# Kernel tuning notes

Measured on AMD Instinct MI355X. Metric: run time of the kernel, lower is better.

Reference implementation:

```python
import jax, jax.numpy as jnp
import numpy as np

B, L, D, H = 2, 1024, 1024, 16
HD = D // H           # 64 head dim
P = 2 * L - 1         # 2047 relative positions (covers offsets -(L-1)..L-1 with wrap)


def setup_inputs() -> dict:
    key = jax.random.key(0)
    ks = jax.random.split(key, 6)
    x = jax.random.normal(ks[0], (B, L, D), dtype=jnp.float32)
    # causal mask: True where attention is disallowed (masked_fill semantics)
    mask = jnp.triu(jnp.ones((L, L), dtype=bool), k=1)
    W_qkv = jax.random.normal(ks[1], (D, 3 * D), dtype=jnp.float32) * 0.02
    b_qkv = jnp.zeros((3 * D,), dtype=jnp.float32)
    W_o = jax.random.normal(ks[2], (D, D), dtype=jnp.float32) * 0.02
    b_o = jnp.zeros((D,), dtype=jnp.float32)
    Er = jax.random.normal(ks[3], (H, P, HD), dtype=jnp.float32)
    return {"x": x, "mask": mask, "W_qkv": W_qkv, "b_qkv": b_qkv,
            "W_o": W_o, "b_o": b_o, "Er": Er}


def reference(x, mask, W_qkv, b_qkv, W_o, b_o, Er):
    b, l, d = x.shape
    h, p, hd = Er.shape
    qkv = x @ W_qkv + b_qkv                              # [b, l, 3d]
    q, k, v = jnp.split(qkv, 3, axis=-1)
    q = q.reshape(b, l, h, hd).transpose(0, 2, 1, 3)     # [b, h, l, hd]
    k = k.reshape(b, l, h, hd).transpose(0, 2, 1, 3)
    v = v.reshape(b, l, h, hd).transpose(0, 2, 1, 3)

    scale = 1.0 / jnp.sqrt(jnp.float32(hd))
    a = jnp.einsum('bhid,bhjd->bhij', q, k) * scale      # [b, h, l, l]

    # relative-position bias: QEr[b,h,i,j] = sum_d q[b,h,i,d] * Er[h, (j-i)%p, d]
    # Efficient skew form: contract q with full table, then gather along last axis.
    QE = jnp.einsum('bhid,hpd->bhip', q, Er)             # [b, h, l, p]
    rel = (jnp.arange(l)[None, :] - jnp.arange(l)[:, None]) % p  # [l, l], matches torch neg-index wrap
    QEr = jnp.take_along_axis(QE, rel[None, None], axis=-1)      # [b, h, l, l]
    a = a + QEr

    a = jnp.where(mask, -jnp.inf, a)
    a = jax.nn.softmax(a, axis=-1)                        # dropout is identity in eval

    out = jnp.einsum('bhij,bhjd->bihd', a, v).reshape(b, l, d)
    return out @ W_o + b_o
```

## Files before the change

### kernel.cpp

```cpp
#include <hip/hip_runtime.h>

typedef _Float16 f16;
typedef _Float16 f16x8 __attribute__((ext_vector_type(8)));
typedef float f32x4 __attribute__((ext_vector_type(4)));

static_assert(sizeof(f16x8) == 16, "f16x8 must be 16B");

#define MFMA16x16x32F(a, b, c) __builtin_amdgcn_mfma_f32_16x16x32_f16((a), (b), (c), 0, 0, 0)

#define NB 2
#define NL 1024
#define ND 1024
#define NH 16
#define NHD 64
#define NP 2047
#define NBH (NB * NH)

__device__ __forceinline__ void wave_sync_lds() {
  __builtin_amdgcn_sched_barrier(0);
  asm volatile("s_waitcnt lgkmcnt(0)" ::: "memory");
  __builtin_amdgcn_sched_barrier(0);
}

__device__ __forceinline__ void gload16(const f16* g, f16* lds) {
  __builtin_amdgcn_global_load_lds((const __attribute__((address_space(1))) void*)g,
                                   (__attribute__((address_space(3))) void*)lds, 16, 0, 0);
}

__global__ __launch_bounds__(256) void prep_all_k(const float* __restrict__ er,
                                                  f16* __restrict__ epf,
                                                  const float* __restrict__ x,
                                                  f16* __restrict__ xf,
                                                  const float* __restrict__ Wqkv,
                                                  f16* __restrict__ WTqkv,
                                                  const float* __restrict__ Wo,
                                                  f16* __restrict__ WTo) {
  const int b = blockIdx.x;
  const int t = threadIdx.x;
  if (b < 8192) {
    const int i = b * 256 + t;
    const int e = i & 7;
    const int lane = (i >> 3) & 63;
    const int half = (i >> 9) & 1;
    const int ob = (i >> 10) & 127;
    const int h = i >> 17;
    const int g = lane >> 4, cl = lane & 15;
    const int o = ob * 16 - 1024 + cl;
    const int p = (o <= 0) ? -o : (NP - o);
    const int d = half * 32 + g * 8 + e;
    epf[i] = (f16)er[(size_t)(h * NP + p) * NHD + d];
  } else if (b < 16384) {
    const int i = (b - 8192) * 256 + t;
    xf[i] = (f16)x[i];
  } else {
    __shared__ float tile[64][68];
    const int b2 = b - 16384;
    const int bx = b2 >> 4;
    const int k0 = (b2 & 15) * 64;
    const float* W;
    f16* WT;
    int N, n0;
    if (bx < 48) { W = Wqkv; WT = WTqkv; N = 3072; n0 = bx * 64; }
    else         { W = Wo;   WT = WTo;   N = 1024; n0 = (bx - 48) * 64; }
    const int rc = t & 15;
    const int rr0 = t >> 4;
#pragma unroll
    for (int i = 0; i < 4; ++i) {
      const int row = rr0 + i * 16;
      float4 v = *(const float4*)(W + (size_t)(k0 + row) * N + n0 + rc * 4);
      *(float4*)&tile[row][rc * 4] = v;
    }
    __syncthreads();
    const int n = t >> 2, kc = (t & 3) * 16;
    f16x8 h0, h1;
#pragma unroll
    for (int e = 0; e < 8; ++e) h0[e] = (f16)tile[kc + e][n];
#pragma unroll
    for (int e = 0; e < 8; ++e) h1[e] = (f16)tile[kc + 8 + e][n];
    f16* dst = WT + (size_t)(n0 + n) * ND + k0 + kc;
    *(f16x8*)dst = h0;
    *(f16x8*)(dst + 8) = h1;
  }
}

__global__ __launch_bounds__(256) void qkv_gemm_k(const f16* __restrict__ Xf,
                                                  const f16* __restrict__ WT,
                                                  const float* __restrict__ bias,
                                                  f16* __restrict__ qf,
                                                  f16* __restrict__ kp, f16* __restrict__ vp) {
  __shared__ f16 sA[2][64 * 32], sB[2][128 * 32];
  const int t = threadIdx.x;
  const int lane = t & 63;
  const int w = t >> 6;
  const int cl = lane & 15;
  const int g = lane >> 4;
  const int m0 = blockIdx.y * 64;
  const int n0 = blockIdx.x * 128;

  const int arow = w * 16 + (lane >> 2);
  const int brow0 = w * 32 + (lane >> 2);
  const int scol = ((lane & 3) ^ ((lane >> 3) & 3)) * 8;
  const int rsw = (g ^ ((cl >> 1) & 3)) * 8;

  f32x4 acc[4][2] = {};

  for (int k0 = 0; k0 < ND; k0 += 64) {
#pragma unroll
    for (int kc = 0; kc < 2; ++kc) {
      const int kk = k0 + kc * 32;
      gload16(Xf + (size_t)(m0 + arow) * ND + kk + scol, &sA[kc][w * 512]);
      const f16* gb0 = WT + (size_t)(n0 + brow0) * ND + kk + scol;
      gload16(gb0, &sB[kc][w * 1024]);
      gload16(gb0 + (size_t)16 * ND, &sB[kc][w * 1024 + 512]);
    }
    __syncthreads();

#pragma unroll
    for (int kc = 0; kc < 2; ++kc) {
      f16x8 ah[4], bh[2];
#pragma unroll
      for (int fm = 0; fm < 4; ++fm) ah[fm] = *(const f16x8*)&sA[kc][(fm * 16 + cl) * 32 + rsw];
#pragma unroll
      for (int fn = 0; fn < 2; ++fn) bh[fn] = *(const f16x8*)&sB[kc][(w * 32 + fn * 16 + cl) * 32 + rsw];
#pragma unroll
      for (int fm = 0; fm < 4; ++fm)
#pragma unroll
        for (int fn = 0; fn < 2; ++fn)
          acc[fm][fn] = MFMA16x16x32F(ah[fm], bh[fn], acc[fm][fn]);
    }
    __syncthreads();
  }

#pragma unroll
  for (int fm = 0; fm < 4; ++fm) {
#pragma unroll
    for (int fn = 0; fn < 2; ++fn) {
#pragma unroll
      for (int reg = 0; reg < 4; ++reg) {
        const int gm = m0 + fm * 16 + g * 4 + reg;
        const int gn = n0 + w * 32 + fn * 16 + cl;
        float val = acc[fm][fn][reg] + bias[gn];
        const int bb = gm >> 10, lpos = gm & 1023;
        const int sec = gn >> 10, hc = gn & 1023;
        const int hh = hc >> 6, dd = hc & 63;
        const int bh = bb * NH + hh;
        if (sec == 0) {
          qf[(size_t)(bh * NL + lpos) * NHD + dd] = (f16)val;
        } else if (sec == 1) {
          const size_t idx = ((size_t)((bh * 64 + (lpos >> 4)) * 2 + (dd >> 5))) * 512 +
                             ((((dd >> 3) & 3) << 4) + (lpos & 15)) * 8 + (dd & 7);
          kp[idx] = (f16)val;
        } else {
          const size_t idx = ((size_t)(((bh * 16 + (lpos >> 6)) * 4 + (dd >> 4)) * 2 +
                                       ((lpos >> 5) & 1))) * 512 +
                             ((((lpos >> 3) & 3) << 4) + (dd & 15)) * 8 + (lpos & 7);
          vp[idx] = (f16)val;
        }
      }
    }
  }
}

__global__ __launch_bounds__(256) void attn_k(const f16* __restrict__ qf,
                                              const f16* __restrict__ kp, const f16* __restrict__ vp,
                                              const f16* __restrict__ epf,
                                              f16* __restrict__ ao) {
  __shared__ float s_lds[4][16][67];
  __shared__ float mb[4][16], lbuf[4][16], linv[16];

  const int t = threadIdx.x;
  const int w = t >> 6;
  const int lane = t & 63;
  const int cl = lane & 15;
  const int g = lane >> 4;

  const int n = blockIdx.x;
  const int xcd = n & 7, idx = n >> 3;
  const int bh = (xcd << 2) | (idx >> 6);
  const int itile = 63 - (idx & 63);
  const int i0 = itile * 16;
  const int h = bh & (NH - 1);
  const int nchunks = (itile >> 2) + 1;

  const f16* qfb = qf + (size_t)(bh * NL + i0 + cl) * NHD + g * 8;
  const f16x8 q_f0 = *(const f16x8*)qfb;
  const f16x8 q_f1 = *(const f16x8*)(qfb + 32);

  f32x4 acc_o[4] = {};
  float m_s = -3e38f, l_s = 0.0f;

  for (int jc = w; jc < nchunks; jc += 4) {
    const int j0 = jc * 64;
    const int delta = i0 - j0;

    const f16* vbase = vp + ((size_t)(bh * 16 + (j0 >> 6)) * 8) * 512 + lane * 8;
    f16x8 vf[4][2];
#pragma unroll
    for (int t4 = 0; t4 < 4; ++t4) {
      vf[t4][0] = *(const f16x8*)(vbase + (t4 * 2 + 0) * 512);
      vf[t4][1] = *(const f16x8*)(vbase + (t4 * 2 + 1) * 512);
    }

    const f16* kbase = kp + ((size_t)(bh * 64 + (j0 >> 4)) * 2) * 512 + lane * 8;
    f32x4 acc_s[4];
    __builtin_amdgcn_s_setprio(1);
#pragma unroll
    for (int jn = 0; jn < 4; ++jn) {
      f16x8 kf0 = *(const f16x8*)(kbase + (jn * 2 + 0) * 512);
      f16x8 kf1 = *(const f16x8*)(kbase + (jn * 2 + 1) * 512);
      f32x4 a = {};
      a = MFMA16x16x32F(q_f0, kf0, a);
      a = MFMA16x16x32F(q_f1, kf1, a);
      acc_s[jn] = a;
    }

    const int ob0 = (delta >> 4) + 60;
    const f16* ebase = epf + ((size_t)(h * 128 + ob0) * 2) * 512 + lane * 8;
    f32x4 acc_e[5];
#pragma unroll
    for (int tt = 0; tt < 5; ++tt) {
      f16x8 ef0 = *(const f16x8*)(ebase + (tt * 2 + 0) * 512);
      f16x8 ef1 = *(const f16x8*)(ebase + (tt * 2 + 1) * 512);
      f32x4 c = {};
      c = MFMA16x16x32F(q_f0, ef0, c);
      c = MFMA16x16x32F(q_f1, ef1, c);
      acc_e[tt] = c;
    }
    __builtin_amdgcn_s_setprio(0);

#pragma unroll
    for (int reg = 0; reg < 4; ++reg) {
      const int r = g * 4 + reg;
      const int src = (g << 4) | ((r - cl) & 15);
      const bool ge = (r >= cl);
#pragma unroll
      for (int jn = 0; jn < 4; ++jn) {
        float e_hi = __shfl(acc_e[4 - jn][reg], src);
        float e_lo = __shfl(acc_e[3 - jn][reg], src);
        s_lds[w][r][jn * 16 + cl] = fmaf(acc_s[jn][reg], 0.125f, ge ? e_hi : e_lo);
      }
    }
    wave_sync_lds();

    float sv[16];
    float tmax = -3e38f;
#pragma unroll
    for (int cc = 0; cc < 16; ++cc) {
      const int c = (cc < 8) ? (g * 8 + cc) : (32 + g * 8 + (cc - 8));
      float v = s_lds[w][cl][c];
      if (c > delta + cl) v = -3e38f;
      sv[cc] = v;
      tmax = fmaxf(tmax, v);
    }
    tmax = fmaxf(tmax, __shfl_xor(tmax, 16));
    tmax = fmaxf(tmax, __shfl_xor(tmax, 32));
    const float m_new = fmaxf(m_s, tmax);
    const float fsc = __builtin_amdgcn_exp2f((m_s - m_new) * 1.44269504f);
    float psum = 0.0f;
    f16x8 pf0, pf1;
#pragma unroll
    for (int cc = 0; cc < 16; ++cc) {
      float pv = __builtin_amdgcn_exp2f((sv[cc] - m_new) * 1.44269504f);
      psum += pv;
      if (cc < 8) pf0[cc & 7] = (f16)pv;
      else        pf1[cc & 7] = (f16)pv;
    }
    psum += __shfl_xor(psum, 16);
    psum += __shfl_xor(psum, 32);
    l_s = l_s * fsc + psum;
    m_s = m_new;

    float fr[4];
#pragma unroll
    for (int reg = 0; reg < 4; ++reg) fr[reg] = __shfl(fsc, g * 4 + reg);
#pragma unroll
    for (int t4 = 0; t4 < 4; ++t4) {
#pragma unroll
      for (int reg = 0; reg < 4; ++reg) acc_o[t4][reg] *= fr[reg];
    }
    __builtin_amdgcn_s_setprio(1);
#pragma unroll
    for (int t4 = 0; t4 < 4; ++t4) {
      acc_o[t4] = MFMA16x16x32F(pf0, vf[t4][0], acc_o[t4]);
      acc_o[t4] = MFMA16x16x32F(pf1, vf[t4][1], acc_o[t4]);
    }
    __builtin_amdgcn_s_setprio(0);
  }

  if (lane < 16) {
    mb[w][lane] = m_s;
    lbuf[w][lane] = l_s;
  }
  __syncthreads();
  const float M = fmaxf(fmaxf(mb[0][cl], mb[1][cl]), fmaxf(mb[2][cl], mb[3][cl]));
  const float sc = __builtin_amdgcn_exp2f((m_s - M) * 1.44269504f);
  float Lt = 0.0f;
#pragma unroll
  for (int ww = 0; ww < 4; ++ww)
    Lt += lbuf[ww][cl] * __builtin_amdgcn_exp2f((mb[ww][cl] - M) * 1.44269504f);
  if (w == 0 && lane < 16) linv[lane] = 1.0f / Lt;
  float fr2[4];
#pragma unroll
  for (int reg = 0; reg < 4; ++reg) fr2[reg] = __shfl(sc, g * 4 + reg);
#pragma unroll
  for (int t4 = 0; t4 < 4; ++t4) {
#pragma unroll
    for (int reg = 0; reg < 4; ++reg)
      s_lds[w][g * 4 + reg][t4 * 16 + cl] = acc_o[t4][reg] * fr2[reg];
  }
  __syncthreads();
  const int bb = bh >> 4;
#pragma unroll
  for (int rep = 0; rep < 4; ++rep) {
    const int o_ = t + rep * 256;
    const int r = o_ >> 6, c = o_ & 63;
    float s = s_lds[0][r][c] + s_lds[1][r][c] + s_lds[2][r][c] + s_lds[3][r][c];
    ao[(size_t)(bb * NL + i0 + r) * ND + h * NHD + c] = (f16)(s * linv[r]);
  }
}

__global__ __launch_bounds__(256) void out_gemm_k(const f16* __restrict__ A,
                                                  const f16* __restrict__ WT,
                                                  const float* __restrict__ bias,
                                                  float* __restrict__ out) {
  __shared__ f16 sA[2][64 * 32], sB[2][128 * 32];
  const int t = threadIdx.x;
  const int lane = t & 63, w = t >> 6;
  const int cl = lane & 15, g = lane >> 4;
  const int m0 = blockIdx.x * 64;
  const int n0 = blockIdx.y * 128;

  const int arow = w * 16 + (lane >> 2);
  const int brow0 = w * 32 + (lane >> 2);
  const int scol = ((lane & 3) ^ ((lane >> 3) & 3)) * 8;
  const int rsw = (g ^ ((cl >> 1) & 3)) * 8;

  f32x4 acc[4][2] = {};

  for (int k0 = 0; k0 < ND; k0 += 64) {
#pragma unroll
    for (int kc = 0; kc < 2; ++kc) {
      const int kk = k0 + kc * 32;
      gload16(A + (size_t)(m0 + arow) * ND + kk + scol, &sA[kc][w * 512]);
      const f16* gb0 = WT + (size_t)(n0 + brow0) * ND + kk + scol;
      gload16(gb0, &sB[kc][w * 1024]);
      gload16(gb0 + (size_t)16 * ND, &sB[kc][w * 1024 + 512]);
    }
    __syncthreads();
#pragma unroll
    for (int kc = 0; kc < 2; ++kc) {
      f16x8 ah[4], bh[2];
#pragma unroll
      for (int fm = 0; fm < 4; ++fm) ah[fm] = *(const f16x8*)&sA[kc][(fm * 16 + cl) * 32 + rsw];
#pragma unroll
      for (int fn = 0; fn < 2; ++fn) bh[fn] = *(const f16x8*)&sB[kc][(w * 32 + fn * 16 + cl) * 32 + rsw];
#pragma unroll
      for (int fm = 0; fm < 4; ++fm)
#pragma unroll
        for (int fn = 0; fn < 2; ++fn)
          acc[fm][fn] = MFMA16x16x32F(ah[fm], bh[fn], acc[fm][fn]);
    }
    __syncthreads();
  }
#pragma unroll
  for (int fm = 0; fm < 4; ++fm) {
#pragma unroll
    for (int fn = 0; fn < 2; ++fn) {
#pragma unroll
      for (int reg = 0; reg < 4; ++reg) {
        const int gm = m0 + fm * 16 + g * 4 + reg;
        const int gn = n0 + w * 32 + fn * 16 + cl;
        out[(size_t)gm * ND + gn] = acc[fm][fn][reg] + bias[gn];
      }
    }
  }
}

extern "C" void kernel_launch(void* const* d_in, const int* in_sizes, int n_in,
                              void* d_out, int out_size, void* d_ws, size_t ws_size,
                              hipStream_t stream) {
  (void)in_sizes; (void)n_in; (void)out_size; (void)ws_size;
  const float* x = (const float*)d_in[0];
  const float* Wqkv = (const float*)d_in[2];
  const float* bqkv = (const float*)d_in[3];
  const float* Wo = (const float*)d_in[4];
  const float* bo = (const float*)d_in[5];
  const float* Er = (const float*)d_in[6];

  char* ws = (char*)d_ws;
  size_t off = 0;
  auto take = [&](size_t bytes) {
    char* p = ws + off;
    off += (bytes + 255) & ~(size_t)255;
    return p;
  };
  const size_t qkN = (size_t)NBH * NL * NHD;
  const size_t xN = (size_t)NB * NL * ND;
  const size_t erpN = (size_t)NH * 128 * 2 * 512;
  f16* epf = (f16*)take(erpN * 2);
  f16* qfw = (f16*)take(qkN * 2);
  f16* kpw = (f16*)take(qkN * 2);
  f16* vpw = (f16*)take(qkN * 2);
  f16* wqkvt = (f16*)take((size_t)3 * ND * ND * 2);
  f16* wot   = (f16*)take((size_t)ND * ND * 2);
  f16* xf    = (f16*)take(xN * 2);
  f16* aow = wqkvt;

  prep_all_k<<<17408, 256, 0, stream>>>(Er, epf, x, xf, Wqkv, wqkvt, Wo, wot);
  qkv_gemm_k<<<dim3(24, 32), 256, 0, stream>>>(xf, wqkvt, bqkv, qfw, kpw, vpw);
  attn_k<<<2048, 256, 0, stream>>>(qfw, kpw, vpw, epf, aow);
  out_gemm_k<<<dim3(32, 8), 256, 0, stream>>>(aow, wot, bo, (float*)d_out);
}
```

Measured before the change: 85.55 us.

## Process two 16-row query tiles per attention block to reuse K/V/Er loads

Each attention block now handles 32 query rows as two 16-row tiles, so every K, V and relative-position fragment loaded per 64-key chunk feeds both tiles. Adjacent tiles share five of six Er fragments. The grid is halved and per-wave register and LDS use roughly doubles. The cost is lower occupancy, fewer blocks for load balancing, and extra masked work for the first tile on the final diagonal chunk.

Result: slower. 99.55 us (+16.4%).

```diff
diff --git a/kernel.cpp b/kernel.cpp
--- a/kernel.cpp
+++ b/kernel.cpp
@@ -165,8 +165,8 @@
                                               const f16* __restrict__ kp, const f16* __restrict__ vp,
                                               const f16* __restrict__ epf,
                                               f16* __restrict__ ao) {
-  __shared__ float s_lds[4][16][67];
-  __shared__ float mb[4][16], lbuf[4][16], linv[16];
+  __shared__ float s_lds[4][2][16][67];
+  __shared__ float mb[4][2][16], lbuf[4][2][16], linv[2][16];
 
   const int t = threadIdx.x;
   const int w = t >> 6;
@@ -176,57 +176,73 @@
 
   const int n = blockIdx.x;
   const int xcd = n & 7, idx = n >> 3;
-  const int bh = (xcd << 2) | (idx >> 6);
-  const int itile = 63 - (idx & 63);
-  const int i0 = itile * 16;
+  const int bh = (xcd << 2) | (idx >> 5);
+  const int itp = 31 - (idx & 31);
+  const int i0A = itp * 32, i0B = i0A + 16;
   const int h = bh & (NH - 1);
-  const int nchunks = (itile >> 2) + 1;
-
-  const f16* qfb = qf + (size_t)(bh * NL + i0 + cl) * NHD + g * 8;
-  const f16x8 q_f0 = *(const f16x8*)qfb;
-  const f16x8 q_f1 = *(const f16x8*)(qfb + 32);
-
-  f32x4 acc_o[4] = {};
-  float m_s = -3e38f, l_s = 0.0f;
+  const int nchunks = (i0B >> 6) + 1;
+
+  const f16* qAp = qf + (size_t)(bh * NL + i0A + cl) * NHD + g * 8;
+  const f16* qBp = qf + (size_t)(bh * NL + i0B + cl) * NHD + g * 8;
+  const f16x8 q_a0 = *(const f16x8*)qAp;
+  const f16x8 q_a1 = *(const f16x8*)(qAp + 32);
+  const f16x8 q_b0 = *(const f16x8*)qBp;
+  const f16x8 q_b1 = *(const f16x8*)(qBp + 32);
+
+  f32x4 acc_oA[4] = {}, acc_oB[4] = {};
+  float mA = -3e38f, lA = 0.0f, mB = -3e38f, lB = 0.0f;
 
   for (int jc = w; jc < nchunks; jc += 4) {
     const int j0 = jc * 64;
-    const int delta = i0 - j0;
-
-    const f16* vbase = vp + ((size_t)(bh * 16 + (j0 >> 6)) * 8) * 512 + lane * 8;
-    f16x8 vf[4][2];
-#pragma unroll
-    for (int t4 = 0; t4 < 4; ++t4) {
-      vf[t4][0] = *(const f16x8*)(vbase + (t4 * 2 + 0) * 512);
-      vf[t4][1] = *(const f16x8*)(vbase + (t4 * 2 + 1) * 512);
-    }
+    const int deltaA = i0A - j0;
+    const int deltaB = deltaA + 16;
 
     const f16* kbase = kp + ((size_t)(bh * 64 + (j0 >> 4)) * 2) * 512 + lane * 8;
-    f32x4 acc_s[4];
+    f32x4 accsA[4], accsB[4];
     __builtin_amdgcn_s_setprio(1);
 #pragma unroll
     for (int jn = 0; jn < 4; ++jn) {
       f16x8 kf0 = *(const f16x8*)(kbase + (jn * 2 + 0) * 512);
       f16x8 kf1 = *(const f16x8*)(kbase + (jn * 2 + 1) * 512);
       f32x4 a = {};
-      a = MFMA16x16x32F(q_f0, kf0, a);
-      a = MFMA16x16x32F(q_f1, kf1, a);
-      acc_s[jn] = a;
-    }
-
-    const int ob0 = (delta >> 4) + 60;
+      a = MFMA16x16x32F(q_a0, kf0, a);
+      a = MFMA16x16x32F(q_a1, kf1, a);
+      accsA[jn] = a;
+      f32x4 bsum = {};
+      bsum = MFMA16x16x32F(q_b0, kf0, bsum);
+      bsum = MFMA16x16x32F(q_b1, kf1, bsum);
+      accsB[jn] = bsum;
+    }
+
+    const int ob0 = (deltaA >> 4) + 60;
     const f16* ebase = epf + ((size_t)(h * 128 + ob0) * 2) * 512 + lane * 8;
-    f32x4 acc_e[5];
-#pragma unroll
-    for (int tt = 0; tt < 5; ++tt) {
+    f32x4 accEA[5], accEB[5];
+#pragma unroll
+    for (int tt = 0; tt < 6; ++tt) {
       f16x8 ef0 = *(const f16x8*)(ebase + (tt * 2 + 0) * 512);
       f16x8 ef1 = *(const f16x8*)(ebase + (tt * 2 + 1) * 512);
-      f32x4 c = {};
-      c = MFMA16x16x32F(q_f0, ef0, c);
-      c = MFMA16x16x32F(q_f1, ef1, c);
-      acc_e[tt] = c;
+      if (tt < 5) {
+        f32x4 c = {};
+        c = MFMA16x16x32F(q_a0, ef0, c);
+        c = MFMA16x16x32F(q_a1, ef1, c);
+        accEA[tt] = c;
+      }
+      if (tt >= 1) {
+        f32x4 c = {};
+        c = MFMA16x16x32F(q_b0, ef0, c);
+        c = MFMA16x16x32F(q_b1, ef1, c);
+        accEB[tt - 1] = c;
+      }
     }
     __builtin_amdgcn_s_setprio(0);
+
+    const f16* vbase = vp + ((size_t)(bh * 16 + (j0 >> 6)) * 8) * 512 + lane * 8;
+    f16x8 vf[4][2];
+#pragma unroll
+    for (int t4 = 0; t4 < 4; ++t4) {
+      vf[t4][0] = *(const f16x8*)(vbase + (t4 * 2 + 0) * 512);
+      vf[t4][1] = *(const f16x8*)(vbase + (t4 * 2 + 1) * 512);
+    }
 
 #pragma unroll
     for (int reg = 0; reg < 4; ++reg) {
@@ -235,87 +251,159 @@
       const bool ge = (r >= cl);
 #pragma unroll
       for (int jn = 0; jn < 4; ++jn) {
-        float e_hi = __shfl(acc_e[4 - jn][reg], src);
-        float e_lo = __shfl(acc_e[3 - jn][reg], src);
-        s_lds[w][r][jn * 16 + cl] = fmaf(acc_s[jn][reg], 0.125f, ge ? e_hi : e_lo);
+        float eA_hi = __shfl(accEA[4 - jn][reg], src);
+        float eA_lo = __shfl(accEA[3 - jn][reg], src);
+        s_lds[w][0][r][jn * 16 + cl] = fmaf(accsA[jn][reg], 0.125f, ge ? eA_hi : eA_lo);
+        float eB_hi = __shfl(accEB[4 - jn][reg], src);
+        float eB_lo = __shfl(accEB[3 - jn][reg], src);
+        s_lds[w][1][r][jn * 16 + cl] = fmaf(accsB[jn][reg], 0.125f, ge ? eB_hi : eB_lo);
       }
     }
     wave_sync_lds();
 
-    float sv[16];
-    float tmax = -3e38f;
-#pragma unroll
-    for (int cc = 0; cc < 16; ++cc) {
-      const int c = (cc < 8) ? (g * 8 + cc) : (32 + g * 8 + (cc - 8));
-      float v = s_lds[w][cl][c];
-      if (c > delta + cl) v = -3e38f;
-      sv[cc] = v;
-      tmax = fmaxf(tmax, v);
-    }
-    tmax = fmaxf(tmax, __shfl_xor(tmax, 16));
-    tmax = fmaxf(tmax, __shfl_xor(tmax, 32));
-    const float m_new = fmaxf(m_s, tmax);
-    const float fsc = __builtin_amdgcn_exp2f((m_s - m_new) * 1.44269504f);
-    float psum = 0.0f;
-    f16x8 pf0, pf1;
-#pragma unroll
-    for (int cc = 0; cc < 16; ++cc) {
-      float pv = __builtin_amdgcn_exp2f((sv[cc] - m_new) * 1.44269504f);
-      psum += pv;
-      if (cc < 8) pf0[cc & 7] = (f16)pv;
-      else        pf1[cc & 7] = (f16)pv;
-    }
-    psum += __shfl_xor(psum, 16);
-    psum += __shfl_xor(psum, 32);
-    l_s = l_s * fsc + psum;
-    m_s = m_new;
-
-    float fr[4];
-#pragma unroll
-    for (int reg = 0; reg < 4; ++reg) fr[reg] = __shfl(fsc, g * 4 + reg);
+    {
+      float sv[16];
+      float tmax = -3e38f;
+#pragma unroll
+      for (int cc = 0; cc < 16; ++cc) {
+        const int c = (cc < 8) ? (g * 8 + cc) : (32 + g * 8 + (cc - 8));
+        float v = s_lds[w][0][cl][c];
+        if (c > deltaA + cl) v = -3e38f;
+        sv[cc] = v;
+        tmax = fmaxf(tmax, v);
+      }
+      tmax = fmaxf(tmax, __shfl_xor(tmax, 16));
+      tmax = fmaxf(tmax, __shfl_xor(tmax, 32));
+      const float m_new = fmaxf(mA, tmax);
+      const float fsc = __builtin_amdgcn_exp2f((mA - m_new) * 1.44269504f);
+      float psum = 0.0f;
+      f16x8 pf0, pf1;
+#pragma unroll
+      for (int cc = 0; cc < 16; ++cc) {
+        float pv = __builtin_amdgcn_exp2f((sv[cc] - m_new) * 1.44269504f);
+        psum += pv;
+        if (cc < 8) pf0[cc & 7] = (f16)pv;
+        else        pf1[cc & 7] = (f16)pv;
+      }
+      psum += __shfl_xor(psum, 16);
+      psum += __shfl_xor(psum, 32);
+      lA = lA * fsc + psum;
+      mA = m_new;
+      float fr[4];
+#pragma unroll
+      for (int reg = 0; reg < 4; ++reg) fr[reg] = __shfl(fsc, g * 4 + reg);
+#pragma unroll
+      for (int t4 = 0; t4 < 4; ++t4) {
+#pragma unroll
+        for (int reg = 0; reg < 4; ++reg) acc_oA[t4][reg] *= fr[reg];
+      }
+      __builtin_amdgcn_s_setprio(1);
+#pragma unroll
+      for (int t4 = 0; t4 < 4; ++t4) {
+        acc_oA[t4] = MFMA16x16x32F(pf0, vf[t4][0], acc_oA[t4]);
+        acc_oA[t4] = MFMA16x16x32F(pf1, vf[t4][1], acc_oA[t4]);
+      }
+      __builtin_amdgcn_s_setprio(0);
+    }
+
+    {
+      float sv[16];
+      float tmax = -3e38f;
+#pragma unroll
+      for (int cc = 0; cc < 16; ++cc) {
+        const int c = (cc < 8) ? (g * 8 + cc) : (32 + g * 8 + (cc - 8));
+        float v = s_lds[w][1][cl][c];
+        if (c > deltaB + cl) v = -3e38f;
+        sv[cc] = v;
+        tmax = fmaxf(tmax, v);
+      }
+      tmax = fmaxf(tmax, __shfl_xor(tmax, 16));
+      tmax = fmaxf(tmax, __shfl_xor(tmax, 32));
+      const float m_new = fmaxf(mB, tmax);
+      const float fsc = __builtin_amdgcn_exp2f((mB - m_new) * 1.44269504f);
+      float psum = 0.0f;
+      f16x8 pf0, pf1;
+#pragma unroll
+      for (int cc = 0; cc < 16; ++cc) {
+        float pv = __builtin_amdgcn_exp2f((sv[cc] - m_new) * 1.44269504f);
+        psum += pv;
+        if (cc < 8) pf0[cc & 7] = (f16)pv;
+        else        pf1[cc & 7] = (f16)pv;
+      }
+      psum += __shfl_xor(psum, 16);
+      psum += __shfl_xor(psum, 32);
+      lB = lB * fsc + psum;
+      mB = m_new;
+      float fr[4];
+#pragma unroll
+      for (int reg = 0; reg < 4; ++reg) fr[reg] = __shfl(fsc, g * 4 + reg);
+#pragma unroll
+      for (int t4 = 0; t4 < 4; ++t4) {
+#pragma unroll
+        for (int reg = 0; reg < 4; ++reg) acc_oB[t4][reg] *= fr[reg];
+      }
+      __builtin_amdgcn_s_setprio(1);
+#pragma unroll
+      for (int t4 = 0; t4 < 4; ++t4) {
+        acc_oB[t4] = MFMA16x16x32F(pf0, vf[t4][0], acc_oB[t4]);
+        acc_oB[t4] = MFMA16x16x32F(pf1, vf[t4][1], acc_oB[t4]);
+      }
+      __builtin_amdgcn_s_setprio(0);
+    }
+  }
+
+  if (lane < 16) {
+    mb[w][0][lane] = mA;
+    lbuf[w][0][lane] = lA;
+    mb[w][1][lane] = mB;
+    lbuf[w][1][lane] = lB;
+  }
+  __syncthreads();
+  {
+    const float M = fmaxf(fmaxf(mb[0][0][cl], mb[1][0][cl]), fmaxf(mb[2][0][cl], mb[3][0][cl]));
+    const float sc = __builtin_amdgcn_exp2f((mA - M) * 1.44269504f);
+    float Lt = 0.0f;
+#pragma unroll
+    for (int ww = 0; ww < 4; ++ww)
+      Lt += lbuf[ww][0][cl] * __builtin_amdgcn_exp2f((mb[ww][0][cl] - M) * 1.44269504f);
+    if (w == 0 && lane < 16) linv[0][lane] = 1.0f / Lt;
+    float fr2[4];
+#pragma unroll
+    for (int reg = 0; reg < 4; ++reg) fr2[reg] = __shfl(sc, g * 4 + reg);
 #pragma unroll
     for (int t4 = 0; t4 < 4; ++t4) {
 #pragma unroll
-      for (int reg = 0; reg < 4; ++reg) acc_o[t4][reg] *= fr[reg];
-    }
-    __builtin_amdgcn_s_setprio(1);
+      for (int reg = 0; reg < 4; ++reg)
+        s_lds[w][0][g * 4 + reg][t4 * 16 + cl] = acc_oA[t4][reg] * fr2[reg];
+    }
+  }
+  {
+    const float M = fmaxf(fmaxf(mb[0][1][cl], mb[1][1][cl]), fmaxf(mb[2][1][cl], mb[3][1][cl]));
+    const float sc = __builtin_amdgcn_exp2f((mB - M) * 1.44269504f);
+    float Lt = 0.0f;
+#pragma unroll
+    for (int ww = 0; ww < 4; ++ww)
+      Lt += lbuf[ww][1][cl] * __builtin_amdgcn_exp2f((mb[ww][1][cl] - M) * 1.44269504f);
+    if (w == 0 && lane < 16) linv[1][lane] = 1.0f / Lt;
+    float fr2[4];
+#pragma unroll
+    for (int reg = 0; reg < 4; ++reg) fr2[reg] = __shfl(sc, g * 4 + reg);
 #pragma unroll
     for (int t4 = 0; t4 < 4; ++t4) {
-      acc_o[t4] = MFMA16x16x32F(pf0, vf[t4][0], acc_o[t4]);
-      acc_o[t4] = MFMA16x16x32F(pf1, vf[t4][1], acc_o[t4]);
-    }
-    __builtin_amdgcn_s_setprio(0);
-  }
-
-  if (lane < 16) {
-    mb[w][lane] = m_s;
-    lbuf[w][lane] = l_s;
-  }
-  __syncthreads();
-  const float M = fmaxf(fmaxf(mb[0][cl], mb[1][cl]), fmaxf(mb[2][cl], mb[3][cl]));
-  const float sc = __builtin_amdgcn_exp2f((m_s - M) * 1.44269504f);
-  float Lt = 0.0f;
-#pragma unroll
-  for (int ww = 0; ww < 4; ++ww)
-    Lt += lbuf[ww][cl] * __builtin_amdgcn_exp2f((mb[ww][cl] - M) * 1.44269504f);
-  if (w == 0 && lane < 16) linv[lane] = 1.0f / Lt;
-  float fr2[4];
-#pragma unroll
-  for (int reg = 0; reg < 4; ++reg) fr2[reg] = __shfl(sc, g * 4 + reg);
-#pragma unroll
-  for (int t4 = 0; t4 < 4; ++t4) {
-#pragma unroll
-    for (int reg = 0; reg < 4; ++reg)
-      s_lds[w][g * 4 + reg][t4 * 16 + cl] = acc_o[t4][reg] * fr2[reg];
+#pragma unroll
+      for (int reg = 0; reg < 4; ++reg)
+        s_lds[w][1][g * 4 + reg][t4 * 16 + cl] = acc_oB[t4][reg] * fr2[reg];
+    }
   }
   __syncthreads();
   const int bb = bh >> 4;
 #pragma unroll
-  for (int rep = 0; rep < 4; ++rep) {
+  for (int rep = 0; rep < 8; ++rep) {
     const int o_ = t + rep * 256;
-    const int r = o_ >> 6, c = o_ & 63;
-    float s = s_lds[0][r][c] + s_lds[1][r][c] + s_lds[2][r][c] + s_lds[3][r][c];
-    ao[(size_t)(bb * NL + i0 + r) * ND + h * NHD + c] = (f16)(s * linv[r]);
+    const int r32 = o_ >> 6, c = o_ & 63;
+    const int tl = r32 >> 4, r = r32 & 15;
+    float s = s_lds[0][tl][r][c] + s_lds[1][tl][r][c] + s_lds[2][tl][r][c] + s_lds[3][tl][r][c];
+    ao[(size_t)(bb * NL + i0A + r32) * ND + h * NHD + c] = (f16)(s * linv[tl][r]);
   }
 }
 
@@ -408,6 +496,6 @@
 
   prep_all_k<<<17408, 256, 0, stream>>>(Er, epf, x, xf, Wqkv, wqkvt, Wo, wot);
   qkv_gemm_k<<<dim3(24, 32), 256, 0, stream>>>(xf, wqkvt, bqkv, qfw, kpw, vpw);
-  attn_k<<<2048, 256, 0, stream>>>(qfw, kpw, vpw, epf, aow);
+  attn_k<<<1024, 256, 0, stream>>>(qfw, kpw, vpw, epf, aow);
   out_gemm_k<<<dim3(32, 8), 256, 0, stream>>>(aow, wot, bo, (float*)d_out);
 }
```
